# Performance work log

Measured on AMD Instinct MI355X. Metric: run time of the kernel, lower is better.

The kernel has to match this reference:

```python
import jax, jax.numpy as jnp
import numpy as np

B, G, IN, H, OUT = 4096, 8, 512, 1024, 64


def setup_inputs() -> dict:
    key = jax.random.key(0)
    k0, k1, k2, k3 = jax.random.split(key, 4)
    x = jax.random.normal(k0, (B, IN), dtype=jnp.float32)
    gid = jax.random.randint(k1, (B,), 0, G, dtype=jnp.int32)
    # Per-group 2-layer MLP params (Kaiming-ish scaling)
    W1 = jax.random.normal(k2, (G, IN, H), dtype=jnp.float32) / np.sqrt(IN)
    b1 = jnp.zeros((G, H), dtype=jnp.float32)
    W2 = jax.random.normal(k3, (G, H, OUT), dtype=jnp.float32) / np.sqrt(H)
    b2 = jnp.zeros((G, OUT), dtype=jnp.float32)
    return {"x": x, "gid": gid, "W1": W1, "b1": b1, "W2": W2, "b2": b2}


def reference(x, gid, W1, b1, W2, b2):
    # Routed 2-layer MLP: each sample i uses expert head gid[i].
    # Compute all G group GEMMs (grouped-GEMM style), then select the
    # routed row per sample with a one-hot contraction (no [B,IN,H]
    # per-sample weight materialization).
    onehot = jax.nn.one_hot(gid, W1.shape[0], dtype=x.dtype)  # [B, G]
    h_all = jnp.einsum('bi,gih->bgh', x, W1) + b1[None]       # [B, G, H]
    h = jax.nn.relu(jnp.einsum('bgh,bg->bh', h_all, onehot))  # [B, H]
    y_all = jnp.einsum('bh,gho->bgo', h, W2) + b2[None]       # [B, G, OUT]
    y = jnp.einsum('bgo,bg->bo', y_all, onehot)               # [B, OUT]
    return y
```

## Files before the change

kernel.cpp:

```cpp
#include <hip/hip_runtime.h>
#include <hip/hip_bf16.h>

#define B_ 4096
#define G_ 8
#define IN_ 512
#define H_ 1024
#define OUT_ 64
#define MAXT64 72
#define MAXT32 136

typedef float f32x4 __attribute__((ext_vector_type(4)));
typedef __bf16 bf16x8 __attribute__((ext_vector_type(8)));
typedef unsigned short u16x8 __attribute__((ext_vector_type(8)));

__device__ inline unsigned short f2bf(float f) {
  unsigned int u = __builtin_bit_cast(unsigned int, f);
  u += 0x7fffu + ((u >> 16) & 1u);
  return (unsigned short)(u >> 16);
}

__device__ inline u16x8 pack8(float4 a, float4 b) {
  return u16x8{f2bf(a.x), f2bf(a.y), f2bf(a.z), f2bf(a.w),
               f2bf(b.x), f2bf(b.y), f2bf(b.z), f2bf(b.w)};
}

__device__ inline bool tile_lookup(const int* __restrict__ meta, int mt,
                                   int shift, int& g, int& row0, int& start,
                                   int& cnt) {
  int ts = 0;
  bool found = false;
#pragma unroll
  for (int gg = 0; gg < G_; gg++) {
    int s = meta[gg], e = meta[gg + 1];
    int T = (e - s + (1 << shift) - 1) >> shift;
    if (!found && mt >= ts && mt < ts + T) {
      g = gg;
      row0 = (mt - ts) << shift;
      start = s;
      cnt = e - s;
      found = true;
    }
    ts += T;
  }
  return found;
}

__global__ __launch_bounds__(256) void prep_kernel(
    const float* __restrict__ W1, const float* __restrict__ W2,
    const float* __restrict__ x, const int* __restrict__ gid,
    unsigned short* __restrict__ W1t, unsigned short* __restrict__ W2t,
    unsigned short* __restrict__ xb, int* __restrict__ meta,
    int* __restrict__ perm) {
  int b = blockIdx.x;
  int t = threadIdx.x;
  if (b < 4096) {
    __shared__ float tile[32][33];
    int h32 = b & 31, k32 = (b >> 5) & 15, g = b >> 9;
    int kl = t >> 3, nl = (t & 7) * 4;
    const float* src =
        W1 + ((size_t)g * IN_ + k32 * 32 + kl) * H_ + h32 * 32 + nl;
    float4 v = *(const float4*)src;
    tile[kl][nl + 0] = v.x;
    tile[kl][nl + 1] = v.y;
    tile[kl][nl + 2] = v.z;
    tile[kl][nl + 3] = v.w;
    __syncthreads();
    int nl2 = t >> 3, kl2 = (t & 7) * 4;
    ushort4 o;
    o.x = f2bf(tile[kl2 + 0][nl2]);
    o.y = f2bf(tile[kl2 + 1][nl2]);
    o.z = f2bf(tile[kl2 + 2][nl2]);
    o.w = f2bf(tile[kl2 + 3][nl2]);
    *(ushort4*)(W1t + ((size_t)g * H_ + h32 * 32 + nl2) * IN_ + k32 * 32 +
                kl2) = o;
  } else if (b < 4608) {
    __shared__ float tile2[32][33];
    int bb = b - 4096;
    int g = bb >> 6, k32 = (bb >> 1) & 31, n32 = bb & 1;
    int kl = t >> 3, nl = (t & 7) * 4;
    const float* src =
        W2 + ((size_t)g * H_ + k32 * 32 + kl) * OUT_ + n32 * 32 + nl;
    float4 v = *(const float4*)src;
    tile2[kl][nl + 0] = v.x;
    tile2[kl][nl + 1] = v.y;
    tile2[kl][nl + 2] = v.z;
    tile2[kl][nl + 3] = v.w;
    __syncthreads();
    int nl2 = t >> 3, kl2 = (t & 7) * 4;
    ushort4 o;
    o.x = f2bf(tile2[kl2 + 0][nl2]);
    o.y = f2bf(tile2[kl2 + 1][nl2]);
    o.z = f2bf(tile2[kl2 + 2][nl2]);
    o.w = f2bf(tile2[kl2 + 3][nl2]);
    *(ushort4*)(W2t + ((size_t)g * OUT_ + n32 * 32 + nl2) * H_ + k32 * 32 +
                kl2) = o;
  } else if (b < 5632) {
    int bb = b - 4608;
    size_t base = (size_t)bb * 2048 + t * 8;
    float4 v0 = *(const float4*)(x + base);
    float4 v1 = *(const float4*)(x + base + 4);
    *(u16x8*)(xb + base) = pack8(v0, v1);
  } else {
    __shared__ unsigned short lc[G_][256];
    __shared__ int offs_s[G_ + 1];
#pragma unroll
    for (int g = 0; g < G_; g++) lc[g][t] = 0;
    int myg[16];
    const int base = t * 16;
    __syncthreads();
#pragma unroll
    for (int j = 0; j < 16; j++) {
      myg[j] = gid[base + j];
      lc[myg[j]][t]++;
    }
    __syncthreads();
    {
      int g = t >> 5, k = t & 31;
      unsigned short pref[8];
      int s = 0;
#pragma unroll
      for (int j = 0; j < 8; j++) {
        pref[j] = (unsigned short)s;
        s += lc[g][8 * k + j];
      }
      int incl = s;
#pragma unroll
      for (int d = 1; d < 32; d <<= 1) {
        int o = __shfl_up(incl, d, 32);
        if (k >= d) incl += o;
      }
      int excl = incl - s;
      if (k == 31) offs_s[g + 1] = incl;
#pragma unroll
      for (int j = 0; j < 8; j++)
        lc[g][8 * k + j] = (unsigned short)(excl + pref[j]);
    }
    __syncthreads();
    if (t == 0) {
      int o = 0;
      for (int g = 0; g < G_; g++) {
        int c = offs_s[g + 1];
        offs_s[g] = o;
        meta[g] = o;
        o += c;
      }
      offs_s[G_] = o;
      meta[G_] = o;
    }
    __syncthreads();
    int cur[G_];
#pragma unroll
    for (int g = 0; g < G_; g++) cur[g] = offs_s[g] + (int)lc[g][t];
#pragma unroll
    for (int j = 0; j < 16; j++) {
      int g = myg[j];
      perm[cur[g]++] = base + j;
    }
  }
}

__global__ __launch_bounds__(256) void gemm1_kernel(
    const unsigned short* __restrict__ xb,
    const unsigned short* __restrict__ W1t, const float* __restrict__ b1,
    const int* __restrict__ meta, const int* __restrict__ perm,
    unsigned short* __restrict__ hb) {
  int b = blockIdx.x;
  int mt = b >> 4, nt = b & 15;
  int g, row0, start, cnt;
  if (!tile_lookup(meta, mt, 5, g, row0, start, cnt)) return;
  int n0 = nt * 64;

  __shared__ __attribute__((aligned(16))) unsigned short As[2][32 * 64];
  __shared__ __attribute__((aligned(16))) unsigned short Bs[2][64 * 64];
  __shared__ int rows[32];

  int tid = threadIdx.x;
  int lane = tid & 63;
  int wv = tid >> 6;

  if (tid < 32) rows[tid] = perm[start + min(row0 + tid, cnt - 1)];
  __syncthreads();

  int r = tid >> 3, cc = tid & 7;
  const unsigned short* xsrc = xb + (size_t)rows[r] * IN_ + cc * 8;
  int aoff = r * 64 + ((cc ^ (r & 7)) << 3);

  int brow0 = wv * 16 + (lane >> 3);
  int brow1 = brow0 + 8;
  int bsl = lane & 7;
  const unsigned short* bsrc0 = W1t + ((size_t)g * H_ + n0 + brow0) * IN_ +
                                ((bsl ^ (brow0 & 7)) << 3);
  const unsigned short* bsrc1 = W1t + ((size_t)g * H_ + n0 + brow1) * IN_ +
                                ((bsl ^ (brow1 & 7)) << 3);
  int boff0 = wv * 1024 + lane * 8;
  int boff1 = wv * 1024 + 512 + lane * 8;

  int fl = lane & 15, q = lane >> 4;
  int m0 = (wv >> 1) * 16, nw = (wv & 1) * 32;
  int apA = (m0 + fl) * 64;
  int bpA = (nw + fl) * 64;
  int bpB = (nw + 16 + fl) * 64;

  f32x4 acc[2];
  acc[0] = f32x4{0.f, 0.f, 0.f, 0.f};
  acc[1] = f32x4{0.f, 0.f, 0.f, 0.f};

  u16x8 av = *(const u16x8*)(xsrc + 0);
  u16x8 bw0 = *(const u16x8*)(bsrc0 + 0);
  u16x8 bw1 = *(const u16x8*)(bsrc1 + 0);
  *(u16x8*)&As[0][aoff] = av;
  *(u16x8*)&Bs[0][boff0] = bw0;
  *(u16x8*)&Bs[0][boff1] = bw1;
  av = *(const u16x8*)(xsrc + 64);
  bw0 = *(const u16x8*)(bsrc0 + 64);
  bw1 = *(const u16x8*)(bsrc1 + 64);
  __syncthreads();

  for (int it = 0; it < 8; it++) {
    int p = it & 1;
    if (it < 7) {
      *(u16x8*)&As[p ^ 1][aoff] = av;
      *(u16x8*)&Bs[p ^ 1][boff0] = bw0;
      *(u16x8*)&Bs[p ^ 1][boff1] = bw1;
    }
    if (it < 6) {
      int kn = (it + 2) * 64;
      av = *(const u16x8*)(xsrc + kn);
      bw0 = *(const u16x8*)(bsrc0 + kn);
      bw1 = *(const u16x8*)(bsrc1 + kn);
    }
#pragma unroll
    for (int s = 0; s < 2; s++) {
      int off = (((s << 2) + q) ^ (fl & 7)) << 3;
      bf16x8 a0 = *(const bf16x8*)&As[p][apA + off];
      bf16x8 fb0 = *(const bf16x8*)&Bs[p][bpA + off];
      bf16x8 fb1 = *(const bf16x8*)&Bs[p][bpB + off];
      acc[0] = __builtin_amdgcn_mfma_f32_16x16x32_bf16(a0, fb0, acc[0], 0, 0, 0);
      acc[1] = __builtin_amdgcn_mfma_f32_16x16x32_bf16(a0, fb1, acc[1], 0, 0, 0);
    }
    __syncthreads();
  }

#pragma unroll
  for (int ni = 0; ni < 2; ni++) {
    int col = n0 + nw + ni * 16 + fl;
    float bias = b1[g * H_ + col];
#pragma unroll
    for (int rg = 0; rg < 4; rg++) {
      int rl = m0 + q * 4 + rg;
      if (row0 + rl < cnt) {
        float v = fmaxf(acc[ni][rg] + bias, 0.f);
        hb[(size_t)(start + row0 + rl) * H_ + col] = f2bf(v);
      }
    }
  }
}

__global__ __launch_bounds__(256) void gemm2_kernel(
    const unsigned short* __restrict__ hb,
    const unsigned short* __restrict__ W2t, const float* __restrict__ b2,
    const int* __restrict__ meta, const int* __restrict__ perm,
    float* __restrict__ y) {
  int mt = blockIdx.x;
  int g, row0, start, cnt;
  if (!tile_lookup(meta, mt, 6, g, row0, start, cnt)) return;

  __shared__ __attribute__((aligned(16))) unsigned short As2[2][64 * 128];
  __shared__ __attribute__((aligned(16))) unsigned short Bs2[2][64 * 128];
  __shared__ int rows[64];

  int tid = threadIdx.x;
  int lane = tid & 63;
  int wv = tid >> 6;

  if (tid < 64) rows[tid] = perm[start + min(row0 + tid, cnt - 1)];

  int arow_in_op = lane >> 4;
  int asl = lane & 15;
  const unsigned short* asrc[4];
  int adst[4];
#pragma unroll
  for (int j = 0; j < 4; j++) {
    int row = wv * 16 + j * 4 + arow_in_op;
    int cs = asl ^ (row & 7);
    asrc[j] =
        hb + (size_t)(start + min(row0 + row, cnt - 1)) * H_ + (cs << 3);
    adst[j] = (wv * 16 + j * 4) * 128 + lane * 8;
  }

  int bn = tid >> 2, qd = tid & 3;
  const unsigned short* bsrc = W2t + ((size_t)g * OUT_ + bn) * H_ + qd * 32;
  int bdst[4];
#pragma unroll
  for (int j = 0; j < 4; j++) {
    int ch = 4 * qd + j;
    bdst[j] = bn * 128 + ((ch ^ (bn & 7)) << 3);
  }

  int fl = lane & 15, q = lane >> 4;
  int m0 = (wv >> 1) * 32, nw = (wv & 1) * 32;
  int apA = (m0 + fl) * 128;
  int apB = (m0 + 16 + fl) * 128;
  int bpA = (nw + fl) * 128;
  int bpB = (nw + 16 + fl) * 128;

  f32x4 acc[2][2];
#pragma unroll
  for (int i = 0; i < 2; i++)
#pragma unroll
    for (int j = 0; j < 2; j++) acc[i][j] = f32x4{0.f, 0.f, 0.f, 0.f};

  u16x8 av[4], bv[4];
#pragma unroll
  for (int j = 0; j < 4; j++) av[j] = *(const u16x8*)(asrc[j] + 0);
#pragma unroll
  for (int j = 0; j < 4; j++) bv[j] = *(const u16x8*)(bsrc + j * 8);
  __syncthreads();
#pragma unroll
  for (int j = 0; j < 4; j++) *(u16x8*)&As2[0][adst[j]] = av[j];
#pragma unroll
  for (int j = 0; j < 4; j++) *(u16x8*)&Bs2[0][bdst[j]] = bv[j];
#pragma unroll
  for (int j = 0; j < 4; j++) av[j] = *(const u16x8*)(asrc[j] + 128);
#pragma unroll
  for (int j = 0; j < 4; j++) bv[j] = *(const u16x8*)(bsrc + 128 + j * 8);
  __syncthreads();

  for (int it = 0; it < 8; it++) {
    int p = it & 1;
    if (it < 7) {
#pragma unroll
      for (int j = 0; j < 4; j++) *(u16x8*)&As2[p ^ 1][adst[j]] = av[j];
#pragma unroll
      for (int j = 0; j < 4; j++) *(u16x8*)&Bs2[p ^ 1][bdst[j]] = bv[j];
    }
    if (it < 6) {
      int kn = (it + 2) * 128;
#pragma unroll
      for (int j = 0; j < 4; j++) av[j] = *(const u16x8*)(asrc[j] + kn);
#pragma unroll
      for (int j = 0; j < 4; j++)
        bv[j] = *(const u16x8*)(bsrc + kn + j * 8);
    }
#pragma unroll
    for (int s = 0; s < 4; s++) {
      int off = (((s << 2) + q) ^ (fl & 7)) << 3;
      bf16x8 a0 = *(const bf16x8*)&As2[p][apA + off];
      bf16x8 a1 = *(const bf16x8*)&As2[p][apB + off];
      bf16x8 fb0 = *(const bf16x8*)&Bs2[p][bpA + off];
      bf16x8 fb1 = *(const bf16x8*)&Bs2[p][bpB + off];
      acc[0][0] = __builtin_amdgcn_mfma_f32_16x16x32_bf16(a0, fb0, acc[0][0], 0, 0, 0);
      acc[1][0] = __builtin_amdgcn_mfma_f32_16x16x32_bf16(a1, fb0, acc[1][0], 0, 0, 0);
      acc[0][1] = __builtin_amdgcn_mfma_f32_16x16x32_bf16(a0, fb1, acc[0][1], 0, 0, 0);
      acc[1][1] = __builtin_amdgcn_mfma_f32_16x16x32_bf16(a1, fb1, acc[1][1], 0, 0, 0);
    }
    __syncthreads();
  }

#pragma unroll
  for (int ni = 0; ni < 2; ni++) {
    int col = nw + ni * 16 + fl;
    float bias = b2[g * OUT_ + col];
#pragma unroll
    for (int mi = 0; mi < 2; mi++) {
#pragma unroll
      for (int rg = 0; rg < 4; rg++) {
        int rl = m0 + mi * 16 + q * 4 + rg;
        if (row0 + rl < cnt) {
          y[(size_t)rows[rl] * OUT_ + col] = acc[mi][ni][rg] + bias;
        }
      }
    }
  }
}

extern "C" void kernel_launch(void* const* d_in, const int* in_sizes, int n_in,
                              void* d_out, int out_size, void* d_ws,
                              size_t ws_size, hipStream_t stream) {
  const float* x = (const float*)d_in[0];
  const int* gid = (const int*)d_in[1];
  const float* W1 = (const float*)d_in[2];
  const float* b1 = (const float*)d_in[3];
  const float* W2 = (const float*)d_in[4];
  const float* b2 = (const float*)d_in[5];
  float* y = (float*)d_out;

  int* meta = (int*)d_ws;
  int* perm = (int*)((char*)d_ws + 64);
  unsigned short* W1t = (unsigned short*)((char*)d_ws + (1u << 16));
  unsigned short* W2t = (unsigned short*)((char*)d_ws + (16u << 20));
  unsigned short* xb = (unsigned short*)((char*)d_ws + (24u << 20));
  unsigned short* hb = (unsigned short*)((char*)d_ws + (32u << 20));

  prep_kernel<<<5633, 256, 0, stream>>>(W1, W2, x, gid, W1t, W2t, xb, meta,
                                        perm);
  gemm1_kernel<<<MAXT32 * 16, 256, 0, stream>>>(xb, W1t, b1, meta, perm, hb);
  gemm2_kernel<<<MAXT64, 256, 0, stream>>>(hb, W2t, b2, meta, perm, y);
}
```

Baseline: 107.8 us.

## Use direct global-to-LDS loads and retile both grouped GEMMs

Both GEMM kernels now stage tiles with global_load_lds (16-byte direct global-to-LDS loads) instead of loading into registers and then writing to shared memory, with the XOR swizzle moved onto the source addresses. gemm1 grows its tiles from 32x64 to 64x128, so each wave computes a 32x64 block with 8 MFMAs per k-step and gets more reuse per staged byte. gemm2 shrinks its M tile from 64 to 32 to launch more blocks. The aim is to cut register-staging overhead and improve reuse in gemm1 and parallelism in gemm2. The cost is fewer gemm1 blocks, plus reliance on the async LDS load being complete at the existing barriers.

```diff
diff --git a/kernel.cpp b/kernel.cpp
--- a/kernel.cpp
+++ b/kernel.cpp
@@ -22,6 +22,13 @@
 __device__ inline u16x8 pack8(float4 a, float4 b) {
   return u16x8{f2bf(a.x), f2bf(a.y), f2bf(a.z), f2bf(a.w),
                f2bf(b.x), f2bf(b.y), f2bf(b.z), f2bf(b.w)};
+}
+
+__device__ inline void gload16(const void* g, void* l) {
+  __builtin_amdgcn_global_load_lds(
+      (const __attribute__((address_space(1))) void*)(unsigned long long)g,
+      (__attribute__((address_space(3))) void*)(unsigned int)(unsigned long long)l,
+      16, 0, 0);
 }
 
 __device__ inline bool tile_lookup(const int* __restrict__ meta, int mt,
@@ -165,92 +172,97 @@
     const int* __restrict__ meta, const int* __restrict__ perm,
     unsigned short* __restrict__ hb) {
   int b = blockIdx.x;
-  int mt = b >> 4, nt = b & 15;
+  int mt = b >> 3, nt = b & 7;
   int g, row0, start, cnt;
-  if (!tile_lookup(meta, mt, 5, g, row0, start, cnt)) return;
-  int n0 = nt * 64;
-
-  __shared__ __attribute__((aligned(16))) unsigned short As[2][32 * 64];
-  __shared__ __attribute__((aligned(16))) unsigned short Bs[2][64 * 64];
-  __shared__ int rows[32];
+  if (!tile_lookup(meta, mt, 6, g, row0, start, cnt)) return;
+  int n0 = nt * 128;
+
+  __shared__ __attribute__((aligned(16))) unsigned short As[2][64 * 64];
+  __shared__ __attribute__((aligned(16))) unsigned short Bs[2][128 * 64];
+  __shared__ int rows[64];
 
   int tid = threadIdx.x;
   int lane = tid & 63;
   int wv = tid >> 6;
 
-  if (tid < 32) rows[tid] = perm[start + min(row0 + tid, cnt - 1)];
+  if (tid < 64) rows[tid] = perm[start + min(row0 + tid, cnt - 1)];
   __syncthreads();
 
-  int r = tid >> 3, cc = tid & 7;
-  const unsigned short* xsrc = xb + (size_t)rows[r] * IN_ + cc * 8;
-  int aoff = r * 64 + ((cc ^ (r & 7)) << 3);
-
-  int brow0 = wv * 16 + (lane >> 3);
-  int brow1 = brow0 + 8;
-  int bsl = lane & 7;
-  const unsigned short* bsrc0 = W1t + ((size_t)g * H_ + n0 + brow0) * IN_ +
-                                ((bsl ^ (brow0 & 7)) << 3);
-  const unsigned short* bsrc1 = W1t + ((size_t)g * H_ + n0 + brow1) * IN_ +
-                                ((bsl ^ (brow1 & 7)) << 3);
-  int boff0 = wv * 1024 + lane * 8;
-  int boff1 = wv * 1024 + 512 + lane * 8;
+  const unsigned short* asrc[2];
+#pragma unroll
+  for (int j = 0; j < 2; j++) {
+    int pp = j * 2048 + tid * 8;
+    int r = pp >> 6;
+    int cpos = (pp >> 3) & 7;
+    asrc[j] = xb + (size_t)rows[r] * IN_ + ((cpos ^ (r & 7)) << 3);
+  }
+  const unsigned short* bsrc[4];
+#pragma unroll
+  for (int j = 0; j < 4; j++) {
+    int pp = j * 2048 + tid * 8;
+    int r = pp >> 6;
+    int cpos = (pp >> 3) & 7;
+    bsrc[j] = W1t + ((size_t)g * H_ + n0 + r) * IN_ + ((cpos ^ (r & 7)) << 3);
+  }
 
   int fl = lane & 15, q = lane >> 4;
-  int m0 = (wv >> 1) * 16, nw = (wv & 1) * 32;
-  int apA = (m0 + fl) * 64;
-  int bpA = (nw + fl) * 64;
-  int bpB = (nw + 16 + fl) * 64;
-
-  f32x4 acc[2];
-  acc[0] = f32x4{0.f, 0.f, 0.f, 0.f};
-  acc[1] = f32x4{0.f, 0.f, 0.f, 0.f};
-
-  u16x8 av = *(const u16x8*)(xsrc + 0);
-  u16x8 bw0 = *(const u16x8*)(bsrc0 + 0);
-  u16x8 bw1 = *(const u16x8*)(bsrc1 + 0);
-  *(u16x8*)&As[0][aoff] = av;
-  *(u16x8*)&Bs[0][boff0] = bw0;
-  *(u16x8*)&Bs[0][boff1] = bw1;
-  av = *(const u16x8*)(xsrc + 64);
-  bw0 = *(const u16x8*)(bsrc0 + 64);
-  bw1 = *(const u16x8*)(bsrc1 + 64);
+  int wm0 = (wv >> 1) * 32, wn0 = (wv & 1) * 64;
+
+  f32x4 acc[2][4];
+#pragma unroll
+  for (int i = 0; i < 2; i++)
+#pragma unroll
+    for (int j = 0; j < 4; j++) acc[i][j] = f32x4{0.f, 0.f, 0.f, 0.f};
+
+  auto stage = [&](int buf, int k0) {
+#pragma unroll
+    for (int j = 0; j < 2; j++)
+      gload16(asrc[j] + k0, &As[buf][j * 2048 + wv * 512]);
+#pragma unroll
+    for (int j = 0; j < 4; j++)
+      gload16(bsrc[j] + k0, &Bs[buf][j * 2048 + wv * 512]);
+  };
+
+  stage(0, 0);
   __syncthreads();
 
   for (int it = 0; it < 8; it++) {
     int p = it & 1;
-    if (it < 7) {
-      *(u16x8*)&As[p ^ 1][aoff] = av;
-      *(u16x8*)&Bs[p ^ 1][boff0] = bw0;
-      *(u16x8*)&Bs[p ^ 1][boff1] = bw1;
-    }
-    if (it < 6) {
-      int kn = (it + 2) * 64;
-      av = *(const u16x8*)(xsrc + kn);
-      bw0 = *(const u16x8*)(bsrc0 + kn);
-      bw1 = *(const u16x8*)(bsrc1 + kn);
-    }
+    if (it < 7) stage(p ^ 1, (it + 1) * 64);
 #pragma unroll
     for (int s = 0; s < 2; s++) {
       int off = (((s << 2) + q) ^ (fl & 7)) << 3;
-      bf16x8 a0 = *(const bf16x8*)&As[p][apA + off];
-      bf16x8 fb0 = *(const bf16x8*)&Bs[p][bpA + off];
-      bf16x8 fb1 = *(const bf16x8*)&Bs[p][bpB + off];
-      acc[0] = __builtin_amdgcn_mfma_f32_16x16x32_bf16(a0, fb0, acc[0], 0, 0, 0);
-      acc[1] = __builtin_amdgcn_mfma_f32_16x16x32_bf16(a0, fb1, acc[1], 0, 0, 0);
-    }
-    __syncthreads();
-  }
-
-#pragma unroll
-  for (int ni = 0; ni < 2; ni++) {
-    int col = n0 + nw + ni * 16 + fl;
+      bf16x8 a0 = *(const bf16x8*)&As[p][(wm0 + fl) * 64 + off];
+      bf16x8 a1 = *(const bf16x8*)&As[p][(wm0 + 16 + fl) * 64 + off];
+      bf16x8 b0 = *(const bf16x8*)&Bs[p][(wn0 + fl) * 64 + off];
+      bf16x8 b1v = *(const bf16x8*)&Bs[p][(wn0 + 16 + fl) * 64 + off];
+      bf16x8 b2v = *(const bf16x8*)&Bs[p][(wn0 + 32 + fl) * 64 + off];
+      bf16x8 b3v = *(const bf16x8*)&Bs[p][(wn0 + 48 + fl) * 64 + off];
+      acc[0][0] = __builtin_amdgcn_mfma_f32_16x16x32_bf16(a0, b0, acc[0][0], 0, 0, 0);
+      acc[0][1] = __builtin_amdgcn_mfma_f32_16x16x32_bf16(a0, b1v, acc[0][1], 0, 0, 0);
+      acc[0][2] = __builtin_amdgcn_mfma_f32_16x16x32_bf16(a0, b2v, acc[0][2], 0, 0, 0);
+      acc[0][3] = __builtin_amdgcn_mfma_f32_16x16x32_bf16(a0, b3v, acc[0][3], 0, 0, 0);
+      acc[1][0] = __builtin_amdgcn_mfma_f32_16x16x32_bf16(a1, b0, acc[1][0], 0, 0, 0);
+      acc[1][1] = __builtin_amdgcn_mfma_f32_16x16x32_bf16(a1, b1v, acc[1][1], 0, 0, 0);
+      acc[1][2] = __builtin_amdgcn_mfma_f32_16x16x32_bf16(a1, b2v, acc[1][2], 0, 0, 0);
+      acc[1][3] = __builtin_amdgcn_mfma_f32_16x16x32_bf16(a1, b3v, acc[1][3], 0, 0, 0);
+    }
+    __syncthreads();
+  }
+
+#pragma unroll
+  for (int ni = 0; ni < 4; ni++) {
+    int col = n0 + wn0 + ni * 16 + fl;
     float bias = b1[g * H_ + col];
 #pragma unroll
-    for (int rg = 0; rg < 4; rg++) {
-      int rl = m0 + q * 4 + rg;
-      if (row0 + rl < cnt) {
-        float v = fmaxf(acc[ni][rg] + bias, 0.f);
-        hb[(size_t)(start + row0 + rl) * H_ + col] = f2bf(v);
+    for (int mi = 0; mi < 2; mi++) {
+#pragma unroll
+      for (int rg = 0; rg < 4; rg++) {
+        int rl = wm0 + mi * 16 + q * 4 + rg;
+        if (row0 + rl < cnt) {
+          float v = fmaxf(acc[mi][ni][rg] + bias, 0.f);
+          hb[(size_t)(start + row0 + rl) * H_ + col] = f2bf(v);
+        }
       }
     }
   }
@@ -263,112 +275,79 @@
     float* __restrict__ y) {
   int mt = blockIdx.x;
   int g, row0, start, cnt;
-  if (!tile_lookup(meta, mt, 6, g, row0, start, cnt)) return;
-
-  __shared__ __attribute__((aligned(16))) unsigned short As2[2][64 * 128];
+  if (!tile_lookup(meta, mt, 5, g, row0, start, cnt)) return;
+
+  __shared__ __attribute__((aligned(16))) unsigned short As2[2][32 * 128];
   __shared__ __attribute__((aligned(16))) unsigned short Bs2[2][64 * 128];
-  __shared__ int rows[64];
+  __shared__ int rows[32];
 
   int tid = threadIdx.x;
   int lane = tid & 63;
   int wv = tid >> 6;
 
-  if (tid < 64) rows[tid] = perm[start + min(row0 + tid, cnt - 1)];
-
-  int arow_in_op = lane >> 4;
-  int asl = lane & 15;
-  const unsigned short* asrc[4];
-  int adst[4];
+  if (tid < 32) rows[tid] = perm[start + min(row0 + tid, cnt - 1)];
+
+  const unsigned short* asrc[2];
+#pragma unroll
+  for (int j = 0; j < 2; j++) {
+    int pp = j * 2048 + tid * 8;
+    int r = pp >> 7;
+    int cpos = (pp >> 3) & 15;
+    asrc[j] = hb + (size_t)(start + min(row0 + r, cnt - 1)) * H_ +
+              ((cpos ^ (r & 7)) << 3);
+  }
+  const unsigned short* bsrc[4];
 #pragma unroll
   for (int j = 0; j < 4; j++) {
-    int row = wv * 16 + j * 4 + arow_in_op;
-    int cs = asl ^ (row & 7);
-    asrc[j] =
-        hb + (size_t)(start + min(row0 + row, cnt - 1)) * H_ + (cs << 3);
-    adst[j] = (wv * 16 + j * 4) * 128 + lane * 8;
-  }
-
-  int bn = tid >> 2, qd = tid & 3;
-  const unsigned short* bsrc = W2t + ((size_t)g * OUT_ + bn) * H_ + qd * 32;
-  int bdst[4];
-#pragma unroll
-  for (int j = 0; j < 4; j++) {
-    int ch = 4 * qd + j;
-    bdst[j] = bn * 128 + ((ch ^ (bn & 7)) << 3);
+    int pp = j * 2048 + tid * 8;
+    int r = pp >> 7;
+    int cpos = (pp >> 3) & 15;
+    bsrc[j] = W2t + ((size_t)g * OUT_ + r) * H_ + ((cpos ^ (r & 7)) << 3);
   }
 
   int fl = lane & 15, q = lane >> 4;
-  int m0 = (wv >> 1) * 32, nw = (wv & 1) * 32;
-  int apA = (m0 + fl) * 128;
-  int apB = (m0 + 16 + fl) * 128;
-  int bpA = (nw + fl) * 128;
-  int bpB = (nw + 16 + fl) * 128;
-
-  f32x4 acc[2][2];
-#pragma unroll
-  for (int i = 0; i < 2; i++)
-#pragma unroll
-    for (int j = 0; j < 2; j++) acc[i][j] = f32x4{0.f, 0.f, 0.f, 0.f};
-
-  u16x8 av[4], bv[4];
-#pragma unroll
-  for (int j = 0; j < 4; j++) av[j] = *(const u16x8*)(asrc[j] + 0);
-#pragma unroll
-  for (int j = 0; j < 4; j++) bv[j] = *(const u16x8*)(bsrc + j * 8);
-  __syncthreads();
-#pragma unroll
-  for (int j = 0; j < 4; j++) *(u16x8*)&As2[0][adst[j]] = av[j];
-#pragma unroll
-  for (int j = 0; j < 4; j++) *(u16x8*)&Bs2[0][bdst[j]] = bv[j];
-#pragma unroll
-  for (int j = 0; j < 4; j++) av[j] = *(const u16x8*)(asrc[j] + 128);
-#pragma unroll
-  for (int j = 0; j < 4; j++) bv[j] = *(const u16x8*)(bsrc + 128 + j * 8);
+  int wm0 = (wv >> 1) * 16, wn0 = (wv & 1) * 32;
+
+  f32x4 acc[2];
+  acc[0] = f32x4{0.f, 0.f, 0.f, 0.f};
+  acc[1] = f32x4{0.f, 0.f, 0.f, 0.f};
+
+  auto stage = [&](int buf, int k0) {
+#pragma unroll
+    for (int j = 0; j < 2; j++)
+      gload16(asrc[j] + k0, &As2[buf][j * 2048 + wv * 512]);
+#pragma unroll
+    for (int j = 0; j < 4; j++)
+      gload16(bsrc[j] + k0, &Bs2[buf][j * 2048 + wv * 512]);
+  };
+
+  stage(0, 0);
   __syncthreads();
 
   for (int it = 0; it < 8; it++) {
     int p = it & 1;
-    if (it < 7) {
-#pragma unroll
-      for (int j = 0; j < 4; j++) *(u16x8*)&As2[p ^ 1][adst[j]] = av[j];
-#pragma unroll
-      for (int j = 0; j < 4; j++) *(u16x8*)&Bs2[p ^ 1][bdst[j]] = bv[j];
-    }
-    if (it < 6) {
-      int kn = (it + 2) * 128;
-#pragma unroll
-      for (int j = 0; j < 4; j++) av[j] = *(const u16x8*)(asrc[j] + kn);
-#pragma unroll
-      for (int j = 0; j < 4; j++)
-        bv[j] = *(const u16x8*)(bsrc + kn + j * 8);
-    }
+    if (it < 7) stage(p ^ 1, (it + 1) * 128);
 #pragma unroll
     for (int s = 0; s < 4; s++) {
       int off = (((s << 2) + q) ^ (fl & 7)) << 3;
-      bf16x8 a0 = *(const bf16x8*)&As2[p][apA + off];
-      bf16x8 a1 = *(const bf16x8*)&As2[p][apB + off];
-      bf16x8 fb0 = *(const bf16x8*)&Bs2[p][bpA + off];
-      bf16x8 fb1 = *(const bf16x8*)&Bs2[p][bpB + off];
-      acc[0][0] = __builtin_amdgcn_mfma_f32_16x16x32_bf16(a0, fb0, acc[0][0], 0, 0, 0);
-      acc[1][0] = __builtin_amdgcn_mfma_f32_16x16x32_bf16(a1, fb0, acc[1][0], 0, 0, 0);
-      acc[0][1] = __builtin_amdgcn_mfma_f32_16x16x32_bf16(a0, fb1, acc[0][1], 0, 0, 0);
-      acc[1][1] = __builtin_amdgcn_mfma_f32_16x16x32_bf16(a1, fb1, acc[1][1], 0, 0, 0);
+      bf16x8 a0 = *(const bf16x8*)&As2[p][(wm0 + fl) * 128 + off];
+      bf16x8 b0 = *(const bf16x8*)&Bs2[p][(wn0 + fl) * 128 + off];
+      bf16x8 b1v = *(const bf16x8*)&Bs2[p][(wn0 + 16 + fl) * 128 + off];
+      acc[0] = __builtin_amdgcn_mfma_f32_16x16x32_bf16(a0, b0, acc[0], 0, 0, 0);
+      acc[1] = __builtin_amdgcn_mfma_f32_16x16x32_bf16(a0, b1v, acc[1], 0, 0, 0);
     }
     __syncthreads();
   }
 
 #pragma unroll
   for (int ni = 0; ni < 2; ni++) {
-    int col = nw + ni * 16 + fl;
+    int col = wn0 + ni * 16 + fl;
     float bias = b2[g * OUT_ + col];
 #pragma unroll
-    for (int mi = 0; mi < 2; mi++) {
-#pragma unroll
-      for (int rg = 0; rg < 4; rg++) {
-        int rl = m0 + mi * 16 + q * 4 + rg;
-        if (row0 + rl < cnt) {
-          y[(size_t)rows[rl] * OUT_ + col] = acc[mi][ni][rg] + bias;
-        }
+    for (int rg = 0; rg < 4; rg++) {
+      int rl = wm0 + q * 4 + rg;
+      if (row0 + rl < cnt) {
+        y[(size_t)rows[rl] * OUT_ + col] = acc[ni][rg] + bias;
       }
     }
   }
@@ -394,6 +373,6 @@
 
   prep_kernel<<<5633, 256, 0, stream>>>(W1, W2, x, gid, W1t, W2t, xb, meta,
                                         perm);
-  gemm1_kernel<<<MAXT32 * 16, 256, 0, stream>>>(xb, W1t, b1, meta, perm, hb);
-  gemm2_kernel<<<MAXT64, 256, 0, stream>>>(hb, W2t, b2, meta, perm, y);
-}
+  gemm1_kernel<<<MAXT64 * 8, 256, 0, stream>>>(xb, W1t, b1, meta, perm, hb);
+  gemm2_kernel<<<MAXT32, 256, 0, stream>>>(hb, W2t, b2, meta, perm, y);
+}
```

Measured after the change: 105.8 us. Within noise of the previous version (-1.9%).
